# Performance work log

Hardware: AMD Instinct MI355X
Metric: run time of the kernel (lower is better)

The kernel has to match this reference:

```python
import jax, jax.numpy as jnp
import numpy as np

VOCAB = 25
HIDDEN = 512
B, S = 64, 2048


def setup_inputs() -> dict:
    key = jax.random.key(0)
    ks = jax.random.split(key, 8)
    tokens = jax.random.randint(ks[0], (B, S), 0, VOCAB)
    lengths = jax.random.randint(ks[1], (B,), 1, S + 1)  # pack_padded requires length >= 1
    k = 1.0 / np.sqrt(HIDDEN)
    u = lambda kk, shp: jax.random.uniform(kk, shp, jnp.float32, -k, k)
    return {
        "tokens": tokens,
        "lengths": lengths,
        "W_ih": u(ks[2], (4 * HIDDEN, VOCAB)),   # gate order i,f,g,o (PyTorch)
        "W_hh": u(ks[3], (4 * HIDDEN, HIDDEN)),
        "b_ih": u(ks[4], (4 * HIDDEN,)),
        "b_hh": u(ks[5], (4 * HIDDEN,)),
        "fc_w": u(ks[6], (1, HIDDEN)),
        "fc_b": u(ks[7], (1,)),
    }


def _lstm_last_hidden(x, lengths, W_ih, W_hh, b_ih, b_hh):
    # x: [B,S,V] one-hot; returns h at each sequence's last valid step (packed-LSTM semantics)
    b, s, _ = x.shape
    h0 = jnp.zeros((b, HIDDEN), x.dtype)
    c0 = jnp.zeros((b, HIDDEN), x.dtype)
    # precompute input projections for all steps: [S,B,4H]
    xg = jnp.einsum('bsv,gv->sbg', x, W_ih) + b_ih + b_hh

    def step(carry, inp):
        h, c = carry
        xt, t = inp
        gates = xt + h @ W_hh.T
        i, f, g, o = jnp.split(gates, 4, axis=-1)
        i = jax.nn.sigmoid(i); f = jax.nn.sigmoid(f)
        g = jnp.tanh(g); o = jax.nn.sigmoid(o)
        c_new = f * c + i * g
        h_new = o * jnp.tanh(c_new)
        m = (t < lengths)[:, None]  # freeze state past sequence end
        return (jnp.where(m, h_new, h), jnp.where(m, c_new, c)), None

    (h, _), _ = jax.lax.scan(step, (h0, c0), (xg, jnp.arange(s)))
    return h


def reference(tokens, lengths, W_ih, W_hh, b_ih, b_hh, fc_w, fc_b):
    # sort by length descending, like the torch forward (output stays in sorted order)
    order = jnp.argsort(-lengths)
    toks = tokens[order]
    lens = lengths[order]
    x = jax.nn.one_hot(toks, VOCAB, dtype=jnp.float32)  # fused one-hot (replaces python loop)
    h = _lstm_last_hidden(x, lens, W_ih, W_hh, b_ih, b_hh)
    return h @ fc_w.T + fc_b  # [B,1]
```

## Files before the change

kernel.cpp:

```cpp
#include <hip/hip_runtime.h>


#define VOCAB 25
#define HIDDEN 512
#define BATCH 64
#define SEQ 2048
#define GB 16
#define NG 4
#define WPG 16
#define HSL 32
#define RWG 128
#define NTHREADS 256
#define HGQ (GB * HIDDEN / 2)

typedef short s16x8 __attribute__((ext_vector_type(8)));
typedef float f32x4 __attribute__((ext_vector_type(4)));

__device__ inline unsigned short f2bf(float x) {
  unsigned u = __float_as_uint(x);
  u += 0x7fffu + ((u >> 16) & 1u);
  return (unsigned short)(u >> 16);
}
__device__ inline float sigf(float x) { return 1.0f / (1.0f + __expf(-x)); }
__device__ inline float tanh_fast(float x) { return 2.0f / (1.0f + __expf(-2.0f * x)) - 1.0f; }

__global__ void prep_kernel(unsigned long long* hg, float* out) {
  const int i = blockIdx.x * blockDim.x + threadIdx.x;
  const int n = blockDim.x * gridDim.x;
  for (int k = i; k < 2 * NG * HGQ; k += n) hg[k] = 0ull;
  if (i < BATCH) out[i] = 0.f;
}

__global__ __launch_bounds__(NTHREADS, 1) void lstm_persistent(
    const int* __restrict__ tokens, const int* __restrict__ lengths,
    const float* __restrict__ W_ih, const float* __restrict__ W_hh,
    const float* __restrict__ b_ih, const float* __restrict__ b_hh,
    const float* __restrict__ fc_w, const float* __restrict__ fc_b,
    float* __restrict__ out, unsigned long long* hg) {
  const int tid = threadIdx.x;
  const int bid = blockIdx.x;
  const int x = bid & 7;
  const int g = x >> 1;
  const int w = ((bid >> 3) << 1) | (x & 1);

  __shared__ __align__(16) unsigned short hbuf[GB][HIDDEN + 8];
  __shared__ float gatesb[GB][RWG + 4];
  __shared__ float xgt[VOCAB][RWG + 4];
  __shared__ int lenAll[BATCH];
  __shared__ int order_[BATCH];
  __shared__ int gIdx[GB];
  __shared__ int gLen[GB];

  if (tid < BATCH) lenAll[tid] = lengths[tid];
  __syncthreads();
  if (tid < BATCH) {
    const int L = lenAll[tid];
    int r = 0;
    for (int j = 0; j < BATCH; ++j) {
      const int lj = lenAll[j];
      r += ((lj > L) || (lj == L && j < tid)) ? 1 : 0;
    }
    order_[r] = tid;
  }
  __syncthreads();
  if (tid < GB) {
    const int oi = order_[g * GB + tid];
    gIdx[tid] = oi;
    gLen[tid] = lenAll[oi];
  }
  for (int i = tid; i < GB * (HIDDEN + 8); i += NTHREADS)
    ((unsigned short*)hbuf)[i] = 0;
  for (int i = tid; i < VOCAB * RWG; i += NTHREADS) {
    const int v = i / RWG, rl = i % RWG;
    const int rg = (rl >> 5) * HIDDEN + w * HSL + (rl & 31);
    xgt[v][rl] = W_ih[rg * VOCAB + v] + b_ih[rg] + b_hh[rg];
  }
  __syncthreads();

  const int T = gLen[0];
  const int lane = tid & 63;
  const int wv = tid >> 6;
  const int m16 = lane & 15;
  const int quad = lane >> 4;

  s16x8 Bf[2][16];
#pragma unroll
  for (int nti = 0; nti < 2; ++nti) {
    const int nt = wv + 4 * nti;
    const int rl = nt * 16 + m16;
    const int rg = (rl >> 5) * HIDDEN + w * HSL + (rl & 31);
    const float* wr = W_hh + (size_t)rg * HIDDEN;
#pragma unroll
    for (int kt = 0; kt < 16; ++kt) {
      const float* p = wr + kt * 32 + quad * 8;
#pragma unroll
      for (int e = 0; e < 8; ++e) Bf[nti][kt][e] = (short)f2bf(p[e]);
    }
  }

  const int cb = tid >> 4;
  const int cs = tid & 15;
  const int jj0 = 2 * cs, jj1 = 2 * cs + 1;
  const int myLen = gLen[cb];
  const int* tokRow = tokens + (size_t)gIdx[cb] * SEQ;
  unsigned long long* const base0 = hg + (size_t)g * HGQ;
  unsigned long long* const base1 = hg + (size_t)(NG + g) * HGQ;

  float c0 = 0.f, c1 = 0.f, h0 = 0.f, h1 = 0.f;

  for (int t = 0; t < T; ++t) {
    const int tok = tokRow[t];

    if (t > 0) {
      const unsigned long long* src = ((t & 1) ? base1 : base0) + tid;
      unsigned long long qA[16], qB[16];
#pragma unroll
      for (int r = 0; r < 16; ++r)
        qA[r] = __hip_atomic_load(src + r * 256, __ATOMIC_RELAXED,
                                  __HIP_MEMORY_SCOPE_AGENT);
      bool useA = true;
      for (;;) {
#pragma unroll
        for (int r = 0; r < 16; ++r)
          qB[r] = __hip_atomic_load(src + r * 256, __ATOMIC_RELAXED,
                                    __HIP_MEMORY_SCOPE_AGENT);
        bool ok = true;
#pragma unroll
        for (int r = 0; r < 16; ++r) ok &= ((unsigned)(qA[r] >> 32) == (unsigned)t);
        if (ok) { useA = true; break; }
#pragma unroll
        for (int r = 0; r < 16; ++r)
          qA[r] = __hip_atomic_load(src + r * 256, __ATOMIC_RELAXED,
                                    __HIP_MEMORY_SCOPE_AGENT);
        ok = true;
#pragma unroll
        for (int r = 0; r < 16; ++r) ok &= ((unsigned)(qB[r] >> 32) == (unsigned)t);
        if (ok) { useA = false; break; }
        __builtin_amdgcn_s_sleep(1);
      }
#pragma unroll
      for (int r = 0; r < 16; ++r) {
        const unsigned long long qv = useA ? qA[r] : qB[r];
        *(unsigned*)&hbuf[cb][r * 32 + jj0] = (unsigned)qv;
      }
    }
    __syncthreads();

    f32x4 acc0a = {0.f, 0.f, 0.f, 0.f}, acc0b = {0.f, 0.f, 0.f, 0.f};
    f32x4 acc1a = {0.f, 0.f, 0.f, 0.f}, acc1b = {0.f, 0.f, 0.f, 0.f};
#pragma unroll
    for (int kt = 0; kt < 16; kt += 2) {
      const s16x8 A0 = *(const s16x8*)&hbuf[m16][kt * 32 + quad * 8];
      const s16x8 A1 = *(const s16x8*)&hbuf[m16][(kt + 1) * 32 + quad * 8];
      acc0a = __builtin_amdgcn_mfma_f32_16x16x32_bf16(A0, Bf[0][kt], acc0a, 0, 0, 0);
      acc1a = __builtin_amdgcn_mfma_f32_16x16x32_bf16(A0, Bf[1][kt], acc1a, 0, 0, 0);
      acc0b = __builtin_amdgcn_mfma_f32_16x16x32_bf16(A1, Bf[0][kt + 1], acc0b, 0, 0, 0);
      acc1b = __builtin_amdgcn_mfma_f32_16x16x32_bf16(A1, Bf[1][kt + 1], acc1b, 0, 0, 0);
    }
    const f32x4 acc0 = acc0a + acc0b;
    const f32x4 acc1 = acc1a + acc1b;
#pragma unroll
    for (int v = 0; v < 4; ++v) {
      gatesb[quad * 4 + v][wv * 16 + m16] = acc0[v];
      gatesb[quad * 4 + v][(wv + 4) * 16 + m16] = acc1[v];
    }
    __syncthreads();

    const float pi0 = gatesb[cb][jj0] + xgt[tok][jj0];
    const float pf0 = gatesb[cb][32 + jj0] + xgt[tok][32 + jj0];
    const float pg0 = gatesb[cb][64 + jj0] + xgt[tok][64 + jj0];
    const float po0 = gatesb[cb][96 + jj0] + xgt[tok][96 + jj0];
    const float pi1 = gatesb[cb][jj1] + xgt[tok][jj1];
    const float pf1 = gatesb[cb][32 + jj1] + xgt[tok][32 + jj1];
    const float pg1 = gatesb[cb][64 + jj1] + xgt[tok][64 + jj1];
    const float po1 = gatesb[cb][96 + jj1] + xgt[tok][96 + jj1];
    if (t < myLen) {
      const float i0 = sigf(pi0), f0 = sigf(pf0), g0 = tanh_fast(pg0), o0 = sigf(po0);
      c0 = f0 * c0 + i0 * g0;
      h0 = o0 * tanh_fast(c0);
      const float i1 = sigf(pi1), f1 = sigf(pf1), g1 = tanh_fast(pg1), o1 = sigf(po1);
      c1 = f1 * c1 + i1 * g1;
      h1 = o1 * tanh_fast(c1);
    }
    if (t + 1 < T) {
      const unsigned payload = (unsigned)f2bf(h0) | ((unsigned)f2bf(h1) << 16);
      const unsigned long long qv = ((unsigned long long)(unsigned)(t + 1) << 32) | payload;
      unsigned long long* hp = (((t + 1) & 1) ? base1 : base0) + w * 256 + tid;
      __hip_atomic_store(hp, qv, __ATOMIC_RELAXED, __HIP_MEMORY_SCOPE_AGENT);
    }
  }

  float part = h0 * fc_w[w * HSL + jj0] + h1 * fc_w[w * HSL + jj1];
  part += __shfl_down(part, 8, 16);
  part += __shfl_down(part, 4, 16);
  part += __shfl_down(part, 2, 16);
  part += __shfl_down(part, 1, 16);
  if (cs == 0) {
    if (w == 0) part += fc_b[0];
    atomicAdd(&out[g * GB + cb], part);
  }
}

extern "C" void kernel_launch(void* const* d_in, const int* in_sizes, int n_in,
                              void* d_out, int out_size, void* d_ws, size_t ws_size,
                              hipStream_t stream) {
  (void)in_sizes; (void)n_in; (void)out_size; (void)ws_size;
  const int* tokens = (const int*)d_in[0];
  const int* lengths = (const int*)d_in[1];
  const float* W_ih = (const float*)d_in[2];
  const float* W_hh = (const float*)d_in[3];
  const float* b_ih = (const float*)d_in[4];
  const float* b_hh = (const float*)d_in[5];
  const float* fc_w = (const float*)d_in[6];
  const float* fc_b = (const float*)d_in[7];
  float* out = (float*)d_out;
  unsigned long long* hglob = (unsigned long long*)d_ws;

  prep_kernel<<<32, 256, 0, stream>>>(hglob, out);
  lstm_persistent<<<64, NTHREADS, 0, stream>>>(tokens, lengths, W_ih, W_hh, b_ih, b_hh,
                                               fc_w, fc_b, out, hglob);
}
```

Before: 6.265 ms.

## Interleave two batch groups per block to hide cross-block sync latency

Each block now handles two 16-sequence groups (A and B) with interleaved sorted indices instead of one, halving the grid to 32 blocks. While one group's hidden state is being exchanged through global memory, the block computes the other group's step, and it prefetches the partner group's h with atomic loads ahead of the spin-wait. This aims to overlap the inter-block h-exchange latency with MFMA and gate work. The trade-off is that each block does twice the serial work per timestep, and the spin loop no longer sleeps between polls.

After: 8.818 ms. 1.41x slower.

```diff
diff --git a/kernel.cpp b/kernel.cpp
--- a/kernel.cpp
+++ b/kernel.cpp
@@ -15,6 +15,7 @@
 
 typedef short s16x8 __attribute__((ext_vector_type(8)));
 typedef float f32x4 __attribute__((ext_vector_type(4)));
+typedef unsigned long long ull;
 
 __device__ inline unsigned short f2bf(float x) {
   unsigned u = __float_as_uint(x);
@@ -24,7 +25,7 @@
 __device__ inline float sigf(float x) { return 1.0f / (1.0f + __expf(-x)); }
 __device__ inline float tanh_fast(float x) { return 2.0f / (1.0f + __expf(-2.0f * x)) - 1.0f; }
 
-__global__ void prep_kernel(unsigned long long* hg, float* out) {
+__global__ void prep_kernel(ull* hg, float* out) {
   const int i = blockIdx.x * blockDim.x + threadIdx.x;
   const int n = blockDim.x * gridDim.x;
   for (int k = i; k < 2 * NG * HGQ; k += n) hg[k] = 0ull;
@@ -36,20 +37,21 @@
     const float* __restrict__ W_ih, const float* __restrict__ W_hh,
     const float* __restrict__ b_ih, const float* __restrict__ b_hh,
     const float* __restrict__ fc_w, const float* __restrict__ fc_b,
-    float* __restrict__ out, unsigned long long* hg) {
+    float* __restrict__ out, ull* hg) {
   const int tid = threadIdx.x;
   const int bid = blockIdx.x;
-  const int x = bid & 7;
-  const int g = x >> 1;
-  const int w = ((bid >> 3) << 1) | (x & 1);
-
-  __shared__ __align__(16) unsigned short hbuf[GB][HIDDEN + 8];
-  __shared__ float gatesb[GB][RWG + 4];
-  __shared__ float xgt[VOCAB][RWG + 4];
+  const int s = bid & 1;
+  const int w = bid >> 1;
+  const int gidA = 2 * s, gidB = 2 * s + 1;
+
+  __shared__ __align__(16) unsigned short hbufA[GB][HIDDEN + 8];
+  __shared__ __align__(16) unsigned short hbufB[GB][HIDDEN + 8];
+  __shared__ float gatesbA[GB][RWG + 5];
+  __shared__ float gatesbB[GB][RWG + 5];
+  __shared__ float xgt[VOCAB][RWG + 5];
   __shared__ int lenAll[BATCH];
   __shared__ int order_[BATCH];
-  __shared__ int gIdx[GB];
-  __shared__ int gLen[GB];
+  __shared__ int gIdxA[GB], gLenA[GB], gIdxB[GB], gLenB[GB];
 
   if (tid < BATCH) lenAll[tid] = lengths[tid];
   __syncthreads();
@@ -64,12 +66,15 @@
   }
   __syncthreads();
   if (tid < GB) {
-    const int oi = order_[g * GB + tid];
-    gIdx[tid] = oi;
-    gLen[tid] = lenAll[oi];
-  }
-  for (int i = tid; i < GB * (HIDDEN + 8); i += NTHREADS)
-    ((unsigned short*)hbuf)[i] = 0;
+    const int ra = s * 32 + 2 * tid;
+    const int oa = order_[ra], ob = order_[ra + 1];
+    gIdxA[tid] = oa; gLenA[tid] = lenAll[oa];
+    gIdxB[tid] = ob; gLenB[tid] = lenAll[ob];
+  }
+  for (int i = tid; i < GB * (HIDDEN + 8); i += NTHREADS) {
+    ((unsigned short*)hbufA)[i] = 0;
+    ((unsigned short*)hbufB)[i] = 0;
+  }
   for (int i = tid; i < VOCAB * RWG; i += NTHREADS) {
     const int v = i / RWG, rl = i % RWG;
     const int rg = (rl >> 5) * HIDDEN + w * HSL + (rl & 31);
@@ -77,7 +82,8 @@
   }
   __syncthreads();
 
-  const int T = gLen[0];
+  const int TA = gLenA[0];
+  const int TB = gLenB[0];
   const int lane = tid & 63;
   const int wv = tid >> 6;
   const int m16 = lane & 15;
@@ -101,103 +107,203 @@
   const int cb = tid >> 4;
   const int cs = tid & 15;
   const int jj0 = 2 * cs, jj1 = 2 * cs + 1;
-  const int myLen = gLen[cb];
-  const int* tokRow = tokens + (size_t)gIdx[cb] * SEQ;
-  unsigned long long* const base0 = hg + (size_t)g * HGQ;
-  unsigned long long* const base1 = hg + (size_t)(NG + g) * HGQ;
-
-  float c0 = 0.f, c1 = 0.f, h0 = 0.f, h1 = 0.f;
-
-  for (int t = 0; t < T; ++t) {
-    const int tok = tokRow[t];
-
+  const int myLenA = gLenA[cb], myLenB = gLenB[cb];
+  const int* tokRowA = tokens + (size_t)gIdxA[cb] * SEQ;
+  const int* tokRowB = tokens + (size_t)gIdxB[cb] * SEQ;
+  ull* const bA0 = hg + (size_t)gidA * HGQ;
+  ull* const bA1 = hg + (size_t)(NG + gidA) * HGQ;
+  ull* const bB0 = hg + (size_t)gidB * HGQ;
+  ull* const bB1 = hg + (size_t)(NG + gidB) * HGQ;
+
+  ull qA[16], qB[16];
+  float cA0 = 0.f, cA1 = 0.f, hA0 = 0.f, hA1 = 0.f;
+  float cB0 = 0.f, cB1 = 0.f, hB0 = 0.f, hB1 = 0.f;
+
+  for (int t = 0; t < TA; ++t) {
+    const int tokA = tokRowA[t];
     if (t > 0) {
-      const unsigned long long* src = ((t & 1) ? base1 : base0) + tid;
-      unsigned long long qA[16], qB[16];
+      bool ok = true;
+#pragma unroll
+      for (int r = 0; r < 16; ++r) ok &= ((unsigned)(qA[r] >> 32) == (unsigned)t);
+      if (!ok) {
+        const ull* src = ((t & 1) ? bA1 : bA0) + tid;
+        for (;;) {
+          ok = true;
+#pragma unroll
+          for (int r = 0; r < 16; ++r)
+            qA[r] = __hip_atomic_load(src + r * 256, __ATOMIC_RELAXED,
+                                      __HIP_MEMORY_SCOPE_AGENT);
+#pragma unroll
+          for (int r = 0; r < 16; ++r) ok &= ((unsigned)(qA[r] >> 32) == (unsigned)t);
+          if (ok) break;
+        }
+      }
 #pragma unroll
       for (int r = 0; r < 16; ++r)
-        qA[r] = __hip_atomic_load(src + r * 256, __ATOMIC_RELAXED,
+        *(unsigned*)&hbufA[cb][r * 32 + jj0] = (unsigned)qA[r];
+    }
+    __syncthreads();
+    {
+      f32x4 acc0a = {0.f, 0.f, 0.f, 0.f}, acc0b = {0.f, 0.f, 0.f, 0.f};
+      f32x4 acc1a = {0.f, 0.f, 0.f, 0.f}, acc1b = {0.f, 0.f, 0.f, 0.f};
+#pragma unroll
+      for (int kt = 0; kt < 16; kt += 2) {
+        const s16x8 A0 = *(const s16x8*)&hbufA[m16][kt * 32 + quad * 8];
+        const s16x8 A1 = *(const s16x8*)&hbufA[m16][(kt + 1) * 32 + quad * 8];
+        acc0a = __builtin_amdgcn_mfma_f32_16x16x32_bf16(A0, Bf[0][kt], acc0a, 0, 0, 0);
+        acc1a = __builtin_amdgcn_mfma_f32_16x16x32_bf16(A0, Bf[1][kt], acc1a, 0, 0, 0);
+        acc0b = __builtin_amdgcn_mfma_f32_16x16x32_bf16(A1, Bf[0][kt + 1], acc0b, 0, 0, 0);
+        acc1b = __builtin_amdgcn_mfma_f32_16x16x32_bf16(A1, Bf[1][kt + 1], acc1b, 0, 0, 0);
+      }
+      const f32x4 acc0 = acc0a + acc0b;
+      const f32x4 acc1 = acc1a + acc1b;
+#pragma unroll
+      for (int v = 0; v < 4; ++v) {
+        gatesbA[quad * 4 + v][wv * 16 + m16] = acc0[v];
+        gatesbA[quad * 4 + v][(wv + 4) * 16 + m16] = acc1[v];
+      }
+    }
+    __syncthreads();
+    if (t > 0 && t < TB) {
+      const ull* src = ((t & 1) ? bB1 : bB0) + tid;
+#pragma unroll
+      for (int r = 0; r < 16; ++r)
+        qB[r] = __hip_atomic_load(src + r * 256, __ATOMIC_RELAXED,
                                   __HIP_MEMORY_SCOPE_AGENT);
-      bool useA = true;
-      for (;;) {
+    }
+    {
+      const float pi0 = gatesbA[cb][jj0] + xgt[tokA][jj0];
+      const float pf0 = gatesbA[cb][32 + jj0] + xgt[tokA][32 + jj0];
+      const float pg0 = gatesbA[cb][64 + jj0] + xgt[tokA][64 + jj0];
+      const float po0 = gatesbA[cb][96 + jj0] + xgt[tokA][96 + jj0];
+      const float pi1 = gatesbA[cb][jj1] + xgt[tokA][jj1];
+      const float pf1 = gatesbA[cb][32 + jj1] + xgt[tokA][32 + jj1];
+      const float pg1 = gatesbA[cb][64 + jj1] + xgt[tokA][64 + jj1];
+      const float po1 = gatesbA[cb][96 + jj1] + xgt[tokA][96 + jj1];
+      if (t < myLenA) {
+        const float i0 = sigf(pi0), f0 = sigf(pf0), g0 = tanh_fast(pg0), o0 = sigf(po0);
+        cA0 = f0 * cA0 + i0 * g0;
+        hA0 = o0 * tanh_fast(cA0);
+        const float i1 = sigf(pi1), f1 = sigf(pf1), g1 = tanh_fast(pg1), o1 = sigf(po1);
+        cA1 = f1 * cA1 + i1 * g1;
+        hA1 = o1 * tanh_fast(cA1);
+      }
+      if (t + 1 < TA) {
+        const unsigned payload = (unsigned)f2bf(hA0) | ((unsigned)f2bf(hA1) << 16);
+        const ull qv = ((ull)(unsigned)(t + 1) << 32) | payload;
+        ull* hp = (((t + 1) & 1) ? bA1 : bA0) + w * 256 + tid;
+        __hip_atomic_store(hp, qv, __ATOMIC_RELAXED, __HIP_MEMORY_SCOPE_AGENT);
+      }
+    }
+
+    if (t < TB) {
+      const int tokB = tokRowB[t];
+      if (t > 0) {
+        bool ok = true;
+#pragma unroll
+        for (int r = 0; r < 16; ++r) ok &= ((unsigned)(qB[r] >> 32) == (unsigned)t);
+        if (!ok) {
+          const ull* src = ((t & 1) ? bB1 : bB0) + tid;
+          for (;;) {
+            ok = true;
+#pragma unroll
+            for (int r = 0; r < 16; ++r)
+              qB[r] = __hip_atomic_load(src + r * 256, __ATOMIC_RELAXED,
+                                        __HIP_MEMORY_SCOPE_AGENT);
+#pragma unroll
+            for (int r = 0; r < 16; ++r) ok &= ((unsigned)(qB[r] >> 32) == (unsigned)t);
+            if (ok) break;
+          }
+        }
 #pragma unroll
         for (int r = 0; r < 16; ++r)
-          qB[r] = __hip_atomic_load(src + r * 256, __ATOMIC_RELAXED,
-                                    __HIP_MEMORY_SCOPE_AGENT);
-        bool ok = true;
-#pragma unroll
-        for (int r = 0; r < 16; ++r) ok &= ((unsigned)(qA[r] >> 32) == (unsigned)t);
-        if (ok) { useA = true; break; }
+          *(unsigned*)&hbufB[cb][r * 32 + jj0] = (unsigned)qB[r];
+      }
+      __syncthreads();
+      {
+        f32x4 acc0a = {0.f, 0.f, 0.f, 0.f}, acc0b = {0.f, 0.f, 0.f, 0.f};
+        f32x4 acc1a = {0.f, 0.f, 0.f, 0.f}, acc1b = {0.f, 0.f, 0.f, 0.f};
+#pragma unroll
+        for (int kt = 0; kt < 16; kt += 2) {
+          const s16x8 A0 = *(const s16x8*)&hbufB[m16][kt * 32 + quad * 8];
+          const s16x8 A1 = *(const s16x8*)&hbufB[m16][(kt + 1) * 32 + quad * 8];
+          acc0a = __builtin_amdgcn_mfma_f32_16x16x32_bf16(A0, Bf[0][kt], acc0a, 0, 0, 0);
+          acc1a = __builtin_amdgcn_mfma_f32_16x16x32_bf16(A0, Bf[1][kt], acc1a, 0, 0, 0);
+          acc0b = __builtin_amdgcn_mfma_f32_16x16x32_bf16(A1, Bf[0][kt + 1], acc0b, 0, 0, 0);
+          acc1b = __builtin_amdgcn_mfma_f32_16x16x32_bf16(A1, Bf[1][kt + 1], acc1b, 0, 0, 0);
+        }
+        const f32x4 acc0 = acc0a + acc0b;
+        const f32x4 acc1 = acc1a + acc1b;
+#pragma unroll
+        for (int v = 0; v < 4; ++v) {
+          gatesbB[quad * 4 + v][wv * 16 + m16] = acc0[v];
+          gatesbB[quad * 4 + v][(wv + 4) * 16 + m16] = acc1[v];
+        }
+      }
+      __syncthreads();
+      if (t + 1 < TA) {
+        const ull* src = (((t + 1) & 1) ? bA1 : bA0) + tid;
 #pragma unroll
         for (int r = 0; r < 16; ++r)
           qA[r] = __hip_atomic_load(src + r * 256, __ATOMIC_RELAXED,
                                     __HIP_MEMORY_SCOPE_AGENT);
-        ok = true;
-#pragma unroll
-        for (int r = 0; r < 16; ++r) ok &= ((unsigned)(qB[r] >> 32) == (unsigned)t);
-        if (ok) { useA = false; break; }
-        __builtin_amdgcn_s_sleep(1);
-      }
-#pragma unroll
-      for (int r = 0; r < 16; ++r) {
-        const unsigned long long qv = useA ? qA[r] : qB[r];
-        *(unsigned*)&hbuf[cb][r * 32 + jj0] = (unsigned)qv;
-      }
-    }
-    __syncthreads();
-
-    f32x4 acc0a = {0.f, 0.f, 0.f, 0.f}, acc0b = {0.f, 0.f, 0.f, 0.f};
-    f32x4 acc1a = {0.f, 0.f, 0.f, 0.f}, acc1b = {0.f, 0.f, 0.f, 0.f};
-#pragma unroll
-    for (int kt = 0; kt < 16; kt += 2) {
-      const s16x8 A0 = *(const s16x8*)&hbuf[m16][kt * 32 + quad * 8];
-      const s16x8 A1 = *(const s16x8*)&hbuf[m16][(kt + 1) * 32 + quad * 8];
-      acc0a = __builtin_amdgcn_mfma_f32_16x16x32_bf16(A0, Bf[0][kt], acc0a, 0, 0, 0);
-      acc1a = __builtin_amdgcn_mfma_f32_16x16x32_bf16(A0, Bf[1][kt], acc1a, 0, 0, 0);
-      acc0b = __builtin_amdgcn_mfma_f32_16x16x32_bf16(A1, Bf[0][kt + 1], acc0b, 0, 0, 0);
-      acc1b = __builtin_amdgcn_mfma_f32_16x16x32_bf16(A1, Bf[1][kt + 1], acc1b, 0, 0, 0);
-    }
-    const f32x4 acc0 = acc0a + acc0b;
-    const f32x4 acc1 = acc1a + acc1b;
-#pragma unroll
-    for (int v = 0; v < 4; ++v) {
-      gatesb[quad * 4 + v][wv * 16 + m16] = acc0[v];
-      gatesb[quad * 4 + v][(wv + 4) * 16 + m16] = acc1[v];
-    }
-    __syncthreads();
-
-    const float pi0 = gatesb[cb][jj0] + xgt[tok][jj0];
-    const float pf0 = gatesb[cb][32 + jj0] + xgt[tok][32 + jj0];
-    const float pg0 = gatesb[cb][64 + jj0] + xgt[tok][64 + jj0];
-    const float po0 = gatesb[cb][96 + jj0] + xgt[tok][96 + jj0];
-    const float pi1 = gatesb[cb][jj1] + xgt[tok][jj1];
-    const float pf1 = gatesb[cb][32 + jj1] + xgt[tok][32 + jj1];
-    const float pg1 = gatesb[cb][64 + jj1] + xgt[tok][64 + jj1];
-    const float po1 = gatesb[cb][96 + jj1] + xgt[tok][96 + jj1];
-    if (t < myLen) {
-      const float i0 = sigf(pi0), f0 = sigf(pf0), g0 = tanh_fast(pg0), o0 = sigf(po0);
-      c0 = f0 * c0 + i0 * g0;
-      h0 = o0 * tanh_fast(c0);
-      const float i1 = sigf(pi1), f1 = sigf(pf1), g1 = tanh_fast(pg1), o1 = sigf(po1);
-      c1 = f1 * c1 + i1 * g1;
-      h1 = o1 * tanh_fast(c1);
-    }
-    if (t + 1 < T) {
-      const unsigned payload = (unsigned)f2bf(h0) | ((unsigned)f2bf(h1) << 16);
-      const unsigned long long qv = ((unsigned long long)(unsigned)(t + 1) << 32) | payload;
-      unsigned long long* hp = (((t + 1) & 1) ? base1 : base0) + w * 256 + tid;
-      __hip_atomic_store(hp, qv, __ATOMIC_RELAXED, __HIP_MEMORY_SCOPE_AGENT);
-    }
-  }
-
-  float part = h0 * fc_w[w * HSL + jj0] + h1 * fc_w[w * HSL + jj1];
-  part += __shfl_down(part, 8, 16);
-  part += __shfl_down(part, 4, 16);
-  part += __shfl_down(part, 2, 16);
-  part += __shfl_down(part, 1, 16);
-  if (cs == 0) {
-    if (w == 0) part += fc_b[0];
-    atomicAdd(&out[g * GB + cb], part);
+      }
+      {
+        const float pi0 = gatesbB[cb][jj0] + xgt[tokB][jj0];
+        const float pf0 = gatesbB[cb][32 + jj0] + xgt[tokB][32 + jj0];
+        const float pg0 = gatesbB[cb][64 + jj0] + xgt[tokB][64 + jj0];
+        const float po0 = gatesbB[cb][96 + jj0] + xgt[tokB][96 + jj0];
+        const float pi1 = gatesbB[cb][jj1] + xgt[tokB][jj1];
+        const float pf1 = gatesbB[cb][32 + jj1] + xgt[tokB][32 + jj1];
+        const float pg1 = gatesbB[cb][64 + jj1] + xgt[tokB][64 + jj1];
+        const float po1 = gatesbB[cb][96 + jj1] + xgt[tokB][96 + jj1];
+        if (t < myLenB) {
+          const float i0 = sigf(pi0), f0 = sigf(pf0), g0 = tanh_fast(pg0), o0 = sigf(po0);
+          cB0 = f0 * cB0 + i0 * g0;
+          hB0 = o0 * tanh_fast(cB0);
+          const float i1 = sigf(pi1), f1 = sigf(pf1), g1 = tanh_fast(pg1), o1 = sigf(po1);
+          cB1 = f1 * cB1 + i1 * g1;
+          hB1 = o1 * tanh_fast(cB1);
+        }
+        if (t + 1 < TB) {
+          const unsigned payload = (unsigned)f2bf(hB0) | ((unsigned)f2bf(hB1) << 16);
+          const ull qv = ((ull)(unsigned)(t + 1) << 32) | payload;
+          ull* hp = (((t + 1) & 1) ? bB1 : bB0) + w * 256 + tid;
+          __hip_atomic_store(hp, qv, __ATOMIC_RELAXED, __HIP_MEMORY_SCOPE_AGENT);
+        }
+      }
+    } else {
+      if (t + 1 < TA) {
+        const ull* src = (((t + 1) & 1) ? bA1 : bA0) + tid;
+#pragma unroll
+        for (int r = 0; r < 16; ++r)
+          qA[r] = __hip_atomic_load(src + r * 256, __ATOMIC_RELAXED,
+                                    __HIP_MEMORY_SCOPE_AGENT);
+      }
+    }
+  }
+
+  {
+    float part = hA0 * fc_w[w * HSL + jj0] + hA1 * fc_w[w * HSL + jj1];
+    part += __shfl_down(part, 8, 16);
+    part += __shfl_down(part, 4, 16);
+    part += __shfl_down(part, 2, 16);
+    part += __shfl_down(part, 1, 16);
+    if (cs == 0) {
+      if (w == 0) part += fc_b[0];
+      atomicAdd(&out[s * 32 + 2 * cb], part);
+    }
+  }
+  {
+    float part = hB0 * fc_w[w * HSL + jj0] + hB1 * fc_w[w * HSL + jj1];
+    part += __shfl_down(part, 8, 16);
+    part += __shfl_down(part, 4, 16);
+    part += __shfl_down(part, 2, 16);
+    part += __shfl_down(part, 1, 16);
+    if (cs == 0) {
+      if (w == 0) part += fc_b[0];
+      atomicAdd(&out[s * 32 + 2 * cb + 1], part);
+    }
   }
 }
 
@@ -214,9 +320,9 @@
   const float* fc_w = (const float*)d_in[6];
   const float* fc_b = (const float*)d_in[7];
   float* out = (float*)d_out;
-  unsigned long long* hglob = (unsigned long long*)d_ws;
+  ull* hglob = (ull*)d_ws;
 
   prep_kernel<<<32, 256, 0, stream>>>(hglob, out);
-  lstm_persistent<<<64, NTHREADS, 0, stream>>>(tokens, lengths, W_ih, W_hh, b_ih, b_hh,
+  lstm_persistent<<<32, NTHREADS, 0, stream>>>(tokens, lengths, W_ih, W_hh, b_ih, b_hh,
                                                fc_w, fc_b, out, hglob);
 }
```
